# Kernel tuning notes

Hardware: AMD Instinct MI355X
Metric: run time of the kernel (lower is better)

## Reference

```python
import jax, jax.numpy as jnp
import numpy as np

IN_FEATURES = 1024
OUT_FEATURES = 64
DEGREE = 3
NUM_KNOTS = 10
BATCH = 8192
K0 = NUM_KNOTS + DEGREE  # number of basis columns / control points per edge


def b_spline_basis(x, knots, degree):
    """Vectorized Cox-de Boor recursion.
    x: (..., ) values in [0,1]; knots: (K0+1,).
    Returns (..., K0) basis; last `degree` columns are zero-padded (matches
    control_points width of num_knots+degree as in the original module).
    """
    t = knots
    n0 = t.shape[0] - 1  # = K0 degree-0 intervals
    xe = x[..., None]
    basis = ((xe >= t[:-1]) & (xe < t[1:])).astype(x.dtype)  # (..., K0)
    for p in range(1, degree + 1):
        ti = t[: n0 - p]
        tip = t[p:n0]
        ti1 = t[1 : n0 - p + 1]
        tip1 = t[p + 1 : n0 + 1]
        d1 = jnp.where(tip - ti > 0, tip - ti, jnp.ones_like(ti))
        d2 = jnp.where(tip1 - ti1 > 0, tip1 - ti1, jnp.ones_like(ti1))
        left = jnp.where(tip - ti > 0, (xe - ti) / d1, 0.0) * basis[..., : n0 - p]
        right = jnp.where(tip1 - ti1 > 0, (tip1 - xe) / d2, 0.0) * basis[..., 1 : n0 - p + 1]
        new = left + right
        pad = jnp.zeros(x.shape + (p,), x.dtype)
        basis = jnp.concatenate([new, pad], axis=-1)
    return basis


def setup_inputs() -> dict:
    key = jax.random.key(0)
    k1, k2 = jax.random.split(key)
    x = jax.random.uniform(k1, (BATCH, IN_FEATURES), dtype=jnp.float32)
    knots = jnp.linspace(0.0, 1.0, NUM_KNOTS + DEGREE + 1, dtype=jnp.float32)
    control_points = jax.random.normal(k2, (OUT_FEATURES, IN_FEATURES, K0), dtype=jnp.float32)
    return {"x": x, "knots": knots, "control_points": control_points}


def reference(x, knots, control_points):
    # basis: (B, in, K0) computed once per input feature (original recomputes
    # it out_features times inside a double loop -- same math, fused here).
    basis = b_spline_basis(x, knots, DEGREE)
    # outputs[b, o] = sum_j sum_k basis[b, j, k] * control_points[o, j, k]
    return jnp.einsum("bjk,ojk->bo", basis, control_points)
```

## Files before the change

kernel.cpp:

```cpp
#include <hip/hip_runtime.h>
#include <hip/hip_bf16.h>
#include <stdint.h>

#define IN_F   1024
#define OUT_F  64
#define BATCH  8192
#define BM     256
#define NTHR   256
#define JSPLIT 32
#define JPB    (IN_F / JSPLIT)
#define JC     4
#define NCH    (JPB / JC)
#define BT_BYTES  (JC * 2048)
#define X_BYTES   (BM * JC * 4)
#define BUF_BYTES (BT_BYTES + X_BYTES)
#define OUTSZ  (BATCH * OUT_F)

typedef __attribute__((ext_vector_type(8)))  short short8;
typedef __attribute__((ext_vector_type(16))) float f32x16;

__global__ void kan_prep(const float* __restrict__ cp, __hip_bfloat16* __restrict__ bt) {
    int j = blockIdx.x * 4 + (threadIdx.x >> 6);
    int o = threadIdx.x & 63;
    const float* src = cp + ((size_t)o * IN_F + j) * 13;
    float v[16];
#pragma unroll
    for (int k = 0; k < 10; ++k) v[k] = src[k];
#pragma unroll
    for (int k = 10; k < 16; ++k) v[k] = 0.0f;
    __hip_bfloat16* dst = bt + (size_t)j * 1024;
#pragma unroll
    for (int kh = 0; kh < 2; ++kh)
#pragma unroll
        for (int e = 0; e < 8; ++e)
            dst[kh * 512 + o * 8 + e] = __float2bfloat16(v[kh * 8 + e]);
}

__device__ __forceinline__ short8 afrag(float xv, int c0) {
    const float t = xv * 13.0f;
    float uu;
    asm("v_fract_f32 %0, %1" : "=v"(uu) : "v"(t));
    const int m = (int)t;
    const float u2 = uu * uu;
    const float omu = 1.0f - uu;
    const float o2 = omu * omu;
    const float B3 = u2 * (uu * (1.0f / 6.0f));
    const float B0 = o2 * (omu * (1.0f / 6.0f));
    const float B1 = __builtin_fmaf(u2, __builtin_fmaf(uu, 0.5f, -1.0f), 2.0f / 3.0f);
    const float B2 = 1.0f - B0 - B1 - B3;
    uint32_t P01, P23;
    asm("v_cvt_pk_bf16_f32 %0, %1, %2" : "=v"(P01) : "v"(B0), "v"(B1));
    asm("v_cvt_pk_bf16_f32 %0, %1, %2" : "=v"(P23) : "v"(B2), "v"(B3));
    const uint64_t V = ((uint64_t)P23 << 32) | (uint64_t)P01;
    const int p = (m << 4) - c0;
    const uint64_t sl = V << ((uint32_t)p & 63);
    const uint64_t sr = V >> ((uint32_t)(-p) & 63);
    const uint64_t t0 = (p < 0) ? sr : sl;
    const uint64_t q0 = ((uint32_t)(p + 63) < 127u) ? t0 : 0ull;
    const uint64_t t1 = (p < 64) ? sr : sl;
    const uint64_t q1 = ((uint32_t)(p - 16) < 112u) ? t1 : 0ull;
    union { uint64_t q[2]; short8 s; } cv;
    cv.q[0] = q0; cv.q[1] = q1;
    return cv.s;
}

template<bool PART>
__launch_bounds__(NTHR, 4)
__global__ void kan_main(const float* __restrict__ x,
                         const __hip_bfloat16* __restrict__ bt,
                         void* __restrict__ outp) {
    __shared__ __attribute__((aligned(16))) char lds[2 * BUF_BYTES];

    const int tid   = threadIdx.x;
    const int w     = tid >> 6;
    const int lane  = tid & 63;
    const int l31   = lane & 31;
    const int khalf = lane >> 5;
    const int c0    = 48 + (khalf << 7);

    const int r0 = blockIdx.x * BM;
    const int j0 = blockIdx.y * JPB;

    const char*  btg = (const char*)bt + (size_t)j0 * 2048;
    const float* xg  = x + (size_t)(r0 + tid) * IN_F + j0;

    uint4  g0, g1;
    float4 gx;

#define LOAD(ch) do {                                            \
        const char* cb = btg + (ch) * BT_BYTES + tid * 16;       \
        g0 = *(const uint4*)(cb);                                \
        g1 = *(const uint4*)(cb + 4096);                         \
        gx = *(const float4*)(xg + (ch) * JC);                   \
    } while (0)

#define WRITE(boff) do {                                         \
        char* d = lds + (boff) + tid * 16;                       \
        *(uint4*)(d)        = g0;                                \
        *(uint4*)(d + 4096) = g1;                                \
        char* xd = lds + (boff) + BT_BYTES + tid * 4;            \
        *(float*)(xd)        = gx.x;                             \
        *(float*)(xd + 1024) = gx.y;                             \
        *(float*)(xd + 2048) = gx.z;                             \
        *(float*)(xd + 3072) = gx.w;                             \
    } while (0)

    f32x16 acc00, acc01, acc10, acc11;
#pragma unroll
    for (int i = 0; i < 16; ++i) {
        acc00[i] = 0.0f; acc01[i] = 0.0f; acc10[i] = 0.0f; acc11[i] = 0.0f;
    }

    LOAD(0);
    WRITE(0);
    LOAD(1);
    __syncthreads();

    int cur = 0;
#pragma unroll 1
    for (int ch = 0; ch < NCH; ++ch) {
        if (ch + 1 < NCH) WRITE(cur ^ BUF_BYTES);
        if (ch + 2 < NCH) LOAD(ch + 2);

        {
            const char* base = lds + cur;
            const char* xb  = base + BT_BYTES + ((w << 6) + l31) * 4;
            const char* bbb = base + (khalf << 10) + l31 * 16;
#pragma unroll
            for (int jl = 0; jl < JC; ++jl) {
                const short8 b0 = *(const short8*)(bbb + jl * 2048);
                const short8 b1 = *(const short8*)(bbb + jl * 2048 + 512);
                const float xv0 = *(const float*)(xb + jl * 1024);
                const float xv1 = *(const float*)(xb + jl * 1024 + 128);

                const short8 a0 = afrag(xv0, c0);
                const short8 a1 = afrag(xv1, c0);

                acc00 = __builtin_amdgcn_mfma_f32_32x32x16_bf16(a0, b0, acc00, 0, 0, 0);
                acc01 = __builtin_amdgcn_mfma_f32_32x32x16_bf16(a0, b1, acc01, 0, 0, 0);
                acc10 = __builtin_amdgcn_mfma_f32_32x32x16_bf16(a1, b0, acc10, 0, 0, 0);
                acc11 = __builtin_amdgcn_mfma_f32_32x32x16_bf16(a1, b1, acc11, 0, 0, 0);
            }
        }

        if (ch + 1 < NCH) __syncthreads();
        cur ^= BUF_BYTES;
    }
#undef LOAD
#undef WRITE

    if (PART) {
        __hip_bfloat16* op = (__hip_bfloat16*)outp + (size_t)blockIdx.y * OUTSZ;
#pragma unroll
        for (int r = 0; r < 16; ++r) {
            const int crow = (r & 3) + 8 * (r >> 2) + 4 * khalf;
            __hip_bfloat16* p0 = op + (size_t)(r0 + (w << 6) + crow) * OUT_F;
            __hip_bfloat16* p1 = p0 + 32 * OUT_F;
            p0[l31]      = __float2bfloat16(acc00[r]);
            p0[l31 + 32] = __float2bfloat16(acc01[r]);
            p1[l31]      = __float2bfloat16(acc10[r]);
            p1[l31 + 32] = __float2bfloat16(acc11[r]);
        }
    } else {
        float* op = (float*)outp;
#pragma unroll
        for (int r = 0; r < 16; ++r) {
            const int crow = (r & 3) + 8 * (r >> 2) + 4 * khalf;
            float* p0 = op + (size_t)(r0 + (w << 6) + crow) * OUT_F;
            float* p1 = p0 + 32 * OUT_F;
            atomicAdd(p0 + l31,      acc00[r]);
            atomicAdd(p0 + l31 + 32, acc01[r]);
            atomicAdd(p1 + l31,      acc10[r]);
            atomicAdd(p1 + l31 + 32, acc11[r]);
        }
    }
}

__global__ void kan_reduce(const __hip_bfloat16* __restrict__ part,
                           float* __restrict__ out) {
    const int i = (blockIdx.x * 256 + threadIdx.x) * 8;
    float s[8] = {0, 0, 0, 0, 0, 0, 0, 0};
#pragma unroll
    for (int b = 0; b < JSPLIT; ++b) {
        const short8 v = *(const short8*)(part + (size_t)b * OUTSZ + i);
#pragma unroll
        for (int e = 0; e < 8; ++e) {
            union { uint32_t u; float f; } c;
            c.u = ((uint32_t)(uint16_t)v[e]) << 16;
            s[e] += c.f;
        }
    }
    float4 lo = {s[0], s[1], s[2], s[3]}, hi = {s[4], s[5], s[6], s[7]};
    *(float4*)(out + i)     = lo;
    *(float4*)(out + i + 4) = hi;
}

extern "C" void kernel_launch(void* const* d_in, const int* in_sizes, int n_in,
                              void* d_out, int out_size, void* d_ws, size_t ws_size,
                              hipStream_t stream) {
    const float* x  = (const float*)d_in[0];
    const float* cp = (const float*)d_in[2];
    float* out = (float*)d_out;
    __hip_bfloat16* bt   = (__hip_bfloat16*)d_ws;
    __hip_bfloat16* part = (__hip_bfloat16*)((char*)d_ws + 2u * 1024u * 1024u);

    const size_t need = 2u * 1024u * 1024u + (size_t)JSPLIT * OUTSZ * 2u;
    const bool use_part = ws_size >= need;

    kan_prep<<<dim3(IN_F / 4), dim3(256), 0, stream>>>(cp, bt);
    if (use_part) {
        kan_main<true><<<dim3(BATCH / BM, JSPLIT), dim3(NTHR), 0, stream>>>(x, bt, (void*)part);
        kan_reduce<<<dim3(OUTSZ / 2048), dim3(256), 0, stream>>>(part, out);
    } else {
        hipMemsetAsync(d_out, 0, (size_t)out_size * sizeof(float), stream);
        kan_main<false><<<dim3(BATCH / BM, JSPLIT), dim3(NTHR), 0, stream>>>(x, bt, (void*)d_out);
    }
}
```

Before: 48.75 us.

## Stage tiles with direct global-to-LDS loads and triple buffering

Replaces the register-staged global loads and LDS writes with `global_load_lds` DMA loads that go straight into shared memory. The loop moves from double to triple buffering, with a single barrier per chunk. The x tile is now stored row-major, so each thread reads its four x values with one float4 LDS load instead of four scalar loads. This is meant to cut VGPR pressure and VALU/LDS-store instructions and to hide load latency better, at the cost of more LDS per block (36 KB), which could limit occupancy. It also relies on the barrier waiting for the async loads to finish.

```diff
diff --git a/kernel.cpp b/kernel.cpp
--- a/kernel.cpp
+++ b/kernel.cpp
@@ -11,13 +11,21 @@
 #define JPB    (IN_F / JSPLIT)
 #define JC     4
 #define NCH    (JPB / JC)
-#define BT_BYTES  (JC * 2048)
-#define X_BYTES   (BM * JC * 4)
-#define BUF_BYTES (BT_BYTES + X_BYTES)
+#define BT_B   (JC * 2048)
+#define X_B    (BM * JC * 4)
+#define BUF_B  (BT_B + X_B)
+#define NBUF   3
 #define OUTSZ  (BATCH * OUT_F)
 
 typedef __attribute__((ext_vector_type(8)))  short short8;
 typedef __attribute__((ext_vector_type(16))) float f32x16;
+
+__device__ __forceinline__ void gll16(const void* g, void* l) {
+    __builtin_amdgcn_global_load_lds(
+        (const __attribute__((address_space(1))) uint32_t*)g,
+        (__attribute__((address_space(3))) uint32_t*)l,
+        16, 0, 0);
+}
 
 __global__ void kan_prep(const float* __restrict__ cp, __hip_bfloat16* __restrict__ bt) {
     int j = blockIdx.x * 4 + (threadIdx.x >> 6);
@@ -69,7 +77,7 @@
 __global__ void kan_main(const float* __restrict__ x,
                          const __hip_bfloat16* __restrict__ bt,
                          void* __restrict__ outp) {
-    __shared__ __attribute__((aligned(16))) char lds[2 * BUF_BYTES];
+    __shared__ __attribute__((aligned(16))) char lds[NBUF * BUF_B];
 
     const int tid   = threadIdx.x;
     const int w     = tid >> 6;
@@ -81,28 +89,16 @@
     const int r0 = blockIdx.x * BM;
     const int j0 = blockIdx.y * JPB;
 
-    const char*  btg = (const char*)bt + (size_t)j0 * 2048;
-    const float* xg  = x + (size_t)(r0 + tid) * IN_F + j0;
-
-    uint4  g0, g1;
-    float4 gx;
-
-#define LOAD(ch) do {                                            \
-        const char* cb = btg + (ch) * BT_BYTES + tid * 16;       \
-        g0 = *(const uint4*)(cb);                                \
-        g1 = *(const uint4*)(cb + 4096);                         \
-        gx = *(const float4*)(xg + (ch) * JC);                   \
-    } while (0)
-
-#define WRITE(boff) do {                                         \
-        char* d = lds + (boff) + tid * 16;                       \
-        *(uint4*)(d)        = g0;                                \
-        *(uint4*)(d + 4096) = g1;                                \
-        char* xd = lds + (boff) + BT_BYTES + tid * 4;            \
-        *(float*)(xd)        = gx.x;                             \
-        *(float*)(xd + 1024) = gx.y;                             \
-        *(float*)(xd + 2048) = gx.z;                             \
-        *(float*)(xd + 3072) = gx.w;                             \
+    const char* btg = (const char*)bt + (size_t)j0 * 2048 + (size_t)tid * 16;
+    const char* xgt = (const char*)(x + (size_t)(r0 + tid) * IN_F + j0);
+    const int   wofs = w << 10;
+
+#define STAGE(ch, bi) do {                                        \
+        char* base_ = lds + (bi) * BUF_B;                         \
+        const char* gb_ = btg + (size_t)(ch) * BT_B;              \
+        gll16(gb_,        base_ + wofs);                          \
+        gll16(gb_ + 4096, base_ + 4096 + wofs);                   \
+        gll16(xgt + (ch) * (JC * 4), base_ + BT_B + wofs);        \
     } while (0)
 
     f32x16 acc00, acc01, acc10, acc11;
@@ -111,31 +107,31 @@
         acc00[i] = 0.0f; acc01[i] = 0.0f; acc10[i] = 0.0f; acc11[i] = 0.0f;
     }
 
-    LOAD(0);
-    WRITE(0);
-    LOAD(1);
-    __syncthreads();
-
-    int cur = 0;
+    STAGE(0, 0);
+    STAGE(1, 1);
+
+    int bi = 0;
 #pragma unroll 1
     for (int ch = 0; ch < NCH; ++ch) {
-        if (ch + 1 < NCH) WRITE(cur ^ BUF_BYTES);
-        if (ch + 2 < NCH) LOAD(ch + 2);
+        __syncthreads();
+        if (ch + 2 < NCH) {
+            int nb = bi + 2; if (nb >= NBUF) nb -= NBUF;
+            STAGE(ch + 2, nb);
+        }
 
         {
-            const char* base = lds + cur;
-            const char* xb  = base + BT_BYTES + ((w << 6) + l31) * 4;
+            const char* base = lds + bi * BUF_B;
+            float xa0[4], xa1[4];
+            const char* xr = base + BT_B + (((w << 6) + l31) << 4);
+            *(float4*)xa0 = *(const float4*)(xr);
+            *(float4*)xa1 = *(const float4*)(xr + 512);
             const char* bbb = base + (khalf << 10) + l31 * 16;
 #pragma unroll
             for (int jl = 0; jl < JC; ++jl) {
                 const short8 b0 = *(const short8*)(bbb + jl * 2048);
                 const short8 b1 = *(const short8*)(bbb + jl * 2048 + 512);
-                const float xv0 = *(const float*)(xb + jl * 1024);
-                const float xv1 = *(const float*)(xb + jl * 1024 + 128);
-
-                const short8 a0 = afrag(xv0, c0);
-                const short8 a1 = afrag(xv1, c0);
-
+                const short8 a0 = afrag(xa0[jl], c0);
+                const short8 a1 = afrag(xa1[jl], c0);
                 acc00 = __builtin_amdgcn_mfma_f32_32x32x16_bf16(a0, b0, acc00, 0, 0, 0);
                 acc01 = __builtin_amdgcn_mfma_f32_32x32x16_bf16(a0, b1, acc01, 0, 0, 0);
                 acc10 = __builtin_amdgcn_mfma_f32_32x32x16_bf16(a1, b0, acc10, 0, 0, 0);
@@ -143,11 +139,9 @@
             }
         }
 
-        if (ch + 1 < NCH) __syncthreads();
-        cur ^= BUF_BYTES;
-    }
-#undef LOAD
-#undef WRITE
+        bi = (bi + 1 == NBUF) ? 0 : bi + 1;
+    }
+#undef STAGE
 
     if (PART) {
         __hip_bfloat16* op = (__hip_bfloat16*)outp + (size_t)blockIdx.y * OUTSZ;
```

New measurement: 49.67 us. Within noise of the previous version (+1.9%).
